# Kernel optimization log

Hardware: AMD Instinct MI355X
Metric: run time of the kernel (lower is better)

## Reference

```python
import jax, jax.numpy as jnp
import numpy as np

N_CHANNEL = 64
N_BAND = 5
N_CLASS = 2
B = 64
K = 2 * N_CHANNEL  # nodes covered by the fully-connected edge_index


def _w(key, shape):
    fan_in = shape[0] if len(shape) == 2 else int(np.prod(shape[1:]))
    return (jax.random.normal(key, shape, jnp.float32) / np.float32(np.sqrt(fan_in)))


def setup_inputs() -> dict:
    key = jax.random.key(0)
    ks = jax.random.split(key, 22)
    d = {}
    d['x1'] = jax.random.normal(ks[0], (B, K, N_BAND), jnp.float32)
    d['x2'] = jax.random.normal(ks[1], (B, K, K), jnp.float32)
    # GCNConv params (weights stored (in, out); PyG applies linear then aggregates, bias after)
    d['gcn1_w'] = _w(ks[2], (N_BAND, 2 * N_BAND))
    d['gcn1_b'] = 0.01 * jax.random.normal(ks[3], (2 * N_BAND,), jnp.float32)
    d['gcn2_w'] = _w(ks[4], (2 * N_BAND, 1))
    d['gcn2_b'] = 0.01 * jax.random.normal(ks[5], (1,), jnp.float32)
    d['fcg_w'] = _w(ks[6], (K, K))
    d['fcg_b'] = 0.01 * jax.random.normal(ks[7], (K,), jnp.float32)
    d['conv1_w'] = _w(ks[8], (16, 1, 3, 3))   # OIHW
    d['conv1_b'] = 0.01 * jax.random.normal(ks[9], (16,), jnp.float32)
    d['conv2_w'] = _w(ks[10], (16, 16, 3, 3))
    d['conv2_b'] = 0.01 * jax.random.normal(ks[11], (16,), jnp.float32)
    d['fcc_w'] = _w(ks[12], (16 * K * K, K))
    d['fcc_b'] = 0.01 * jax.random.normal(ks[13], (K,), jnp.float32)
    d['fc1_w'] = _w(ks[14], (4 * N_CHANNEL, 2 * N_CHANNEL))
    d['fc1_b'] = 0.01 * jax.random.normal(ks[15], (2 * N_CHANNEL,), jnp.float32)
    d['fc2_w'] = _w(ks[16], (2 * N_CHANNEL, N_CHANNEL))
    d['fc2_b'] = 0.01 * jax.random.normal(ks[17], (N_CHANNEL,), jnp.float32)
    d['fc3_w'] = _w(ks[18], (N_CHANNEL, N_CLASS))
    d['fc3_b'] = 0.01 * jax.random.normal(ks[19], (N_CLASS,), jnp.float32)
    return d


def _gcn(x, W, b):
    # Faithful to original: edge_index is fully connected over the FIRST K rows only.
    # With default self-loops, normalized adjacency over rows [0,K) is (1/K)*ones(K,K)
    # (all degrees = K); every other row has only its self-loop (degree 1 -> identity).
    y = x @ W                                   # (B*N, out)
    y = y.at[:K].set(jnp.mean(y[:K], axis=0))   # broadcast mean over first K rows
    return y + b


def _conv(x, w, b):
    y = jax.lax.conv_general_dilated(x, w, (1, 1), 'SAME',
                                     dimension_numbers=('NCHW', 'OIHW', 'NCHW'))
    return jax.nn.relu(y + b[None, :, None, None])


def reference(x1, x2, gcn1_w, gcn1_b, gcn2_w, gcn2_b, fcg_w, fcg_b,
              conv1_w, conv1_b, conv2_w, conv2_b, fcc_w, fcc_b,
              fc1_w, fc1_b, fc2_w, fc2_b, fc3_w, fc3_b):
    Bn, N, Feat = x1.shape
    # GNN branch (dropout is identity in eval mode)
    h = x1.reshape(Bn * N, Feat)
    h = jax.nn.relu(_gcn(h, gcn1_w, gcn1_b))
    h = jax.nn.relu(_gcn(h, gcn2_w, gcn2_b))
    h = h.reshape(Bn, -1)                       # (B, 2*n_channel)
    g = jax.nn.relu(h @ fcg_w + fcg_b)
    # CNN branch
    c = x2[:, None]                             # (B,1,H,W)
    c = _conv(c, conv1_w, conv1_b)
    c = _conv(c, conv2_w, conv2_b)
    c = c.reshape(Bn, -1)                       # channel-major flatten, same as torch .view
    c = jax.nn.relu(c @ fcc_w + fcc_b)
    # Fusion MLP
    x = jnp.concatenate([c, g], axis=1)
    x = jax.nn.relu(x @ fc1_w + fc1_b)
    x = jax.nn.relu(x @ fc2_w + fc2_b)
    return jax.nn.sigmoid(x @ fc3_w + fc3_b)
```

## Files before the change

kernel.cpp:

```cpp
#include <hip/hip_runtime.h>
#include <hip/hip_bf16.h>


#define NROWS   8192
#define IMG     16384
#define FCC_K   262144
#define FCC_BLOCKS 512
#define FCC_KRANGE 512
#define FCC_CHUNK 128

typedef __attribute__((ext_vector_type(8))) short bf16x8;
typedef __attribute__((ext_vector_type(4))) float f32x4;
typedef __attribute__((ext_vector_type(4))) unsigned short us4;
typedef __attribute__((ext_vector_type(8))) unsigned short us8;

__device__ __forceinline__ unsigned short f2bf(float f) {
    unsigned u = __float_as_uint(f);
    unsigned r = (u + 0x7FFFu + ((u >> 16) & 1u)) >> 16;
    return (unsigned short)r;
}

__device__ __forceinline__ int fcc_swz(int col, int k) {
    return col*128 + (k ^ ((((col >> 2) ^ col) & 15) << 3));
}

__global__ __launch_bounds__(128) void gcnfcg_kernel(
    const float* __restrict__ x1,
    const float* __restrict__ W1,
    const float* __restrict__ b1,
    const float* __restrict__ W2,
    const float* __restrict__ b2,
    const float* __restrict__ fcgW,
    const float* __restrict__ fcgb,
    float* __restrict__ g)
{
    __shared__ float sW1[50], sb1[10], sW2[10], smean[10];
    __shared__ float sy1[128][10];
    __shared__ float sh2[128];
    int b = blockIdx.x, t = threadIdx.x;
    if (t < 50) sW1[t] = W1[t];
    if (t < 10) { sb1[t] = b1[t]; sW2[t] = W2[t]; }
    __syncthreads();

    int r = b*128 + t;
    float x[5];
    #pragma unroll
    for (int f = 0; f < 5; ++f) x[f] = x1[r*5 + f];
    float y[10];
    #pragma unroll
    for (int o = 0; o < 10; ++o) {
        float a = 0.f;
        #pragma unroll
        for (int f = 0; f < 5; ++f) a += x[f] * sW1[f*10 + o];
        y[o] = a;
    }

    float h1row[10];
    if (b == 0) {
        #pragma unroll
        for (int o = 0; o < 10; ++o) sy1[t][o] = y[o];
        __syncthreads();
        if (t < 10) {
            float s = 0.f;
            for (int rr = 0; rr < 128; ++rr) s += sy1[rr][t];
            smean[t] = fmaxf(s * (1.f/128.f) + sb1[t], 0.f);
        }
        __syncthreads();
        #pragma unroll
        for (int o = 0; o < 10; ++o) h1row[o] = smean[o];
    } else {
        #pragma unroll
        for (int o = 0; o < 10; ++o) h1row[o] = fmaxf(y[o] + sb1[o], 0.f);
    }

    float y2 = 0.f;
    #pragma unroll
    for (int o = 0; o < 10; ++o) y2 += h1row[o] * sW2[o];
    sh2[t] = fmaxf(y2 + b2[0], 0.f);
    __syncthreads();

    float acc = fcgb[t];
    #pragma unroll 8
    for (int k = 0; k < 128; ++k) acc += sh2[k] * fcgW[k*128 + t];
    g[b*128 + t] = fmaxf(acc, 0.f);
}

__global__ __launch_bounds__(256) void conv12_kernel(
    const float* __restrict__ x2,
    const float* __restrict__ w1,
    const float* __restrict__ b1,
    const float* __restrict__ w2,
    const float* __restrict__ b2,
    unsigned short* __restrict__ c2bf)
{
    __shared__ float sx2[8][130];
    __shared__ unsigned short sin[6*130*16];
    __shared__ unsigned short sB[5*512];
    __shared__ float sw1[144], sb1v[16];

    int tid = threadIdx.x;
    int blk = blockIdx.x;
    int b   = blk >> 5;
    int R0  = (blk & 31) * 4;

    if (tid < 144) sw1[tid] = w1[tid];
    if (tid < 16)  sb1v[tid] = b1[tid];

    for (int idx = tid; idx < 2560; idx += 256) {
        int q   = idx >> 9;
        int rem = idx & 511;
        int l   = rem >> 3;
        int e   = rem & 7;
        int k   = (l >> 4) * 8 + e;
        int oc  = l & 15;
        int ic  = k & 15;
        int dd  = 2*q + (k >> 4);
        unsigned short bits = 0;
        if (dd < 9) bits = f2bf(w2[oc*144 + ic*9 + dd]);
        sB[idx] = bits;
    }
    if (tid < 192) {
        int rr = tid >> 5, rem = tid & 31;
        int cc = (rem < 16) ? 0 : 129;
        sin[(rr*130 + cc)*16 + (rem & 15)] = 0;
    }
    {
        const float* xb = x2 + (size_t)b * IMG;
        for (int idx = tid; idx < 8*130; idx += 256) {
            int rr = idx / 130, cc = idx - rr*130;
            int ri = R0 - 2 + rr, gj = cc - 1;
            float v = 0.f;
            if (ri >= 0 && ri < 128 && gj >= 0 && gj < 128)
                v = xb[ri*128 + gj];
            sx2[rr][cc] = v;
        }
    }
    __syncthreads();

    for (int p = tid; p < 768; p += 256) {
        int rr = p >> 7;
        int cc = p & 127;
        int ri1 = R0 - 1 + rr;
        bool valid = (ri1 >= 0 && ri1 < 128);
        float in9[3][3];
        #pragma unroll
        for (int di = 0; di < 3; ++di)
          #pragma unroll
          for (int dj = 0; dj < 3; ++dj)
              in9[di][dj] = sx2[rr + di][cc + dj];
        us8 o0, o1;
        #pragma unroll
        for (int oc = 0; oc < 16; ++oc) {
            float acc = sb1v[oc];
            #pragma unroll
            for (int di = 0; di < 3; ++di)
              #pragma unroll
              for (int dj = 0; dj < 3; ++dj)
                  acc += in9[di][dj] * sw1[oc*9 + di*3 + dj];
            unsigned short bits = valid ? f2bf(fmaxf(acc, 0.f)) : (unsigned short)0;
            if (oc < 8) o0[oc] = bits; else o1[oc - 8] = bits;
        }
        unsigned short* dst = &sin[(rr*130 + cc + 1)*16];
        *reinterpret_cast<us8*>(dst)     = o0;
        *reinterpret_cast<us8*>(dst + 8) = o1;
    }
    __syncthreads();

    int lane = tid & 63;
    int wv   = tid >> 6;
    int ln   = lane & 15;
    int g    = lane >> 4;
    int ghalf = g & 1;

    int aoff[5];
    #pragma unroll
    for (int q = 0; q < 5; ++q) {
        int dd = 2*q + (g >> 1);
        if (dd > 8) dd = 8;
        int di = dd / 3, dj = dd % 3;
        aoff[q] = ((wv + di)*130 + ln + dj)*16 + ghalf*8;
    }

    bf16x8 bf[5];
    #pragma unroll
    for (int q = 0; q < 5; ++q)
        bf[q] = *reinterpret_cast<const bf16x8*>(&sB[q*512 + lane*8]);

    float bias_oc = b2[ln];
    int r = R0 + wv;
    unsigned short* outbase = c2bf + ((size_t)b*16 + ln)*IMG + r*128;

    #pragma unroll
    for (int t = 0; t < 8; ++t) {
        f32x4 acc = {0.f, 0.f, 0.f, 0.f};
        #pragma unroll
        for (int q = 0; q < 5; ++q) {
            bf16x8 a = *reinterpret_cast<const bf16x8*>(&sin[aoff[q] + t*256]);
            acc = __builtin_amdgcn_mfma_f32_16x16x32_bf16(a, bf[q], acc, 0, 0, 0);
        }
        int pc = t*16 + g*4;
        us4 pk;
        #pragma unroll
        for (int reg = 0; reg < 4; ++reg)
            pk[reg] = f2bf(fmaxf(acc[reg] + bias_oc, 0.f));
        *reinterpret_cast<us4*>(&outbase[pc]) = pk;
    }
}

__global__ __launch_bounds__(256, 3) void fcc_mfma(
    const unsigned short* __restrict__ c2bf,
    const float* __restrict__ W,
    float* __restrict__ partials)
{
    __shared__ unsigned short sWt[128*128];

    int tid  = threadIdx.x;
    int blk  = blockIdx.x;
    int k0   = blk * FCC_KRANGE;
    int lane = tid & 63, wv = tid >> 6;
    int ln   = lane & 15, g = lane >> 4;

    int q  = tid & 31;
    int kO = tid >> 5;

    f32x4 acc[8];
    #pragma unroll
    for (int j = 0; j < 8; ++j) acc[j] = (f32x4){0.f,0.f,0.f,0.f};

    const float* Wb = W + (size_t)k0 * 128;
    const unsigned short* arow = c2bf + (size_t)(16*wv + ln)*FCC_K + k0 + g*8;

    for (int ci = 0; ci < 4; ++ci) {
        const float* Wc = Wb + (size_t)ci * FCC_CHUNK * 128;
        #pragma unroll
        for (int ko2 = 0; ko2 < 2; ++ko2) {
            int kbase = ko2*64 + kO*8;
            float4 rows[8];
            #pragma unroll
            for (int r = 0; r < 8; ++r)
                rows[r] = *reinterpret_cast<const float4*>(
                    Wc + (size_t)(kbase + r)*128 + q*4);
            us8 vc0, vc1, vc2, vc3;
            #pragma unroll
            for (int r = 0; r < 8; ++r) {
                vc0[r] = f2bf(rows[r].x);
                vc1[r] = f2bf(rows[r].y);
                vc2[r] = f2bf(rows[r].z);
                vc3[r] = f2bf(rows[r].w);
            }
            int col0 = q*4;
            *reinterpret_cast<us8*>(&sWt[fcc_swz(col0+0, kbase)]) = vc0;
            *reinterpret_cast<us8*>(&sWt[fcc_swz(col0+1, kbase)]) = vc1;
            *reinterpret_cast<us8*>(&sWt[fcc_swz(col0+2, kbase)]) = vc2;
            *reinterpret_cast<us8*>(&sWt[fcc_swz(col0+3, kbase)]) = vc3;
        }
        __syncthreads();

        bf16x8 af[4];
        #pragma unroll
        for (int ks = 0; ks < 4; ++ks)
            af[ks] = *reinterpret_cast<const bf16x8*>(arow + ci*FCC_CHUNK + ks*32);

        #pragma unroll
        for (int ks = 0; ks < 4; ++ks) {
            #pragma unroll
            for (int j = 0; j < 8; ++j) {
                int col = j*16 + ln;
                bf16x8 bfrag = *reinterpret_cast<const bf16x8*>(
                    &sWt[fcc_swz(col, ks*32 + g*8)]);
                acc[j] = __builtin_amdgcn_mfma_f32_16x16x32_bf16(af[ks], bfrag, acc[j], 0, 0, 0);
            }
        }
        __syncthreads();
    }

    float* p = partials + (size_t)blk * 8192;
    #pragma unroll
    for (int j = 0; j < 8; ++j)
      #pragma unroll
      for (int reg = 0; reg < 4; ++reg) {
          int m = 16*wv + g*4 + reg;
          p[m*128 + j*16 + ln] = acc[j][reg];
      }
}

__global__ __launch_bounds__(512) void head_kernel(
    const float* __restrict__ partials,
    const float* __restrict__ fccb,
    const float* __restrict__ g,
    const float* __restrict__ w1, const float* __restrict__ bb1,
    const float* __restrict__ w2, const float* __restrict__ bb2,
    const float* __restrict__ w3, const float* __restrict__ bb3,
    float* __restrict__ out)
{
    __shared__ float sred[4][128];
    __shared__ float sx[256], sh[128], s2[64];
    int b = blockIdx.x, t = threadIdx.x;
    int o = t & 127, pr = t >> 7;

    const float* pb = partials + (size_t)pr*8192 + (size_t)b*128 + o;
    float s = 0.f;
    #pragma unroll 8
    for (int p = 0; p < FCC_BLOCKS/4; ++p) s += pb[(size_t)p*4*8192];
    sred[pr][o] = s;
    __syncthreads();

    if (t < 128) {
        sx[t] = fmaxf(sred[0][t] + sred[1][t] + sred[2][t] + sred[3][t]
                      + fccb[t], 0.f);
    } else if (t < 256) {
        sx[t] = g[b*128 + (t - 128)];
    }
    __syncthreads();

    if (t < 128) {
        float acc = bb1[t];
        for (int k = 0; k < 256; ++k) acc += sx[k] * w1[k*128 + t];
        sh[t] = fmaxf(acc, 0.f);
    }
    __syncthreads();
    if (t < 64) {
        float acc = bb2[t];
        for (int k = 0; k < 128; ++k) acc += sh[k] * w2[k*64 + t];
        s2[t] = fmaxf(acc, 0.f);
    }
    __syncthreads();
    if (t < 2) {
        float acc = bb3[t];
        for (int k = 0; k < 64; ++k) acc += s2[k] * w3[k*2 + t];
        out[b*2 + t] = 1.f / (1.f + __expf(-acc));
    }
}

extern "C" void kernel_launch(void* const* d_in, const int* in_sizes, int n_in,
                              void* d_out, int out_size, void* d_ws, size_t ws_size,
                              hipStream_t stream)
{
    const float* x1      = (const float*)d_in[0];
    const float* x2      = (const float*)d_in[1];
    const float* gcn1_w  = (const float*)d_in[2];
    const float* gcn1_b  = (const float*)d_in[3];
    const float* gcn2_w  = (const float*)d_in[4];
    const float* gcn2_b  = (const float*)d_in[5];
    const float* fcg_w   = (const float*)d_in[6];
    const float* fcg_b   = (const float*)d_in[7];
    const float* conv1_w = (const float*)d_in[8];
    const float* conv1_b = (const float*)d_in[9];
    const float* conv2_w = (const float*)d_in[10];
    const float* conv2_b = (const float*)d_in[11];
    const float* fcc_w   = (const float*)d_in[12];
    const float* fcc_b   = (const float*)d_in[13];
    const float* fc1_w   = (const float*)d_in[14];
    const float* fc1_b   = (const float*)d_in[15];
    const float* fc2_w   = (const float*)d_in[16];
    const float* fc2_b   = (const float*)d_in[17];
    const float* fc3_w   = (const float*)d_in[18];
    const float* fc3_b   = (const float*)d_in[19];
    float* out = (float*)d_out;

    float* ws = (float*)d_ws;
    float* g        = ws;
    unsigned short* c2bf = (unsigned short*)(g + 8192);
    float* partials = (float*)(c2bf + 16777216);

    gcnfcg_kernel<<<64, 128, 0, stream>>>(x1, gcn1_w, gcn1_b, gcn2_w, gcn2_b,
                                          fcg_w, fcg_b, g);
    conv12_kernel<<<2048, 256, 0, stream>>>(x2, conv1_w, conv1_b,
                                            conv2_w, conv2_b, c2bf);
    fcc_mfma<<<FCC_BLOCKS, 256, 0, stream>>>(c2bf, fcc_w, partials);
    head_kernel<<<64, 512, 0, stream>>>(partials, fcc_b, g, fc1_w, fc1_b,
                                        fc2_w, fc2_b, fc3_w, fc3_b, out);
}
```

Measured before the change: 96.22 us.

## Double-buffer fcc weight tiles and fold GCN branch into head kernel

The fcc GEMM kernel now processes 64-row chunks with two shared-memory buffers. Each iteration issues the global loads of the next chunk's weights and activations before running the MFMAs on the current chunk, so memory latency overlaps compute. Occupancy is lowered to 2 blocks per CU. Separately, the GCN+fcg kernel is removed and its work is fused into the head kernel, saving one launch and a workspace round trip at the cost of a longer head kernel.

```diff
diff --git a/kernel.cpp b/kernel.cpp
--- a/kernel.cpp
+++ b/kernel.cpp
@@ -7,7 +7,8 @@
 #define FCC_K   262144
 #define FCC_BLOCKS 512
 #define FCC_KRANGE 512
-#define FCC_CHUNK 128
+#define FCC_CHUNK 64
+#define FCC_NCHUNK 8
 
 typedef __attribute__((ext_vector_type(8))) short bf16x8;
 typedef __attribute__((ext_vector_type(4))) float f32x4;
@@ -20,69 +21,8 @@
     return (unsigned short)r;
 }
 
-__device__ __forceinline__ int fcc_swz(int col, int k) {
-    return col*128 + (k ^ ((((col >> 2) ^ col) & 15) << 3));
-}
-
-__global__ __launch_bounds__(128) void gcnfcg_kernel(
-    const float* __restrict__ x1,
-    const float* __restrict__ W1,
-    const float* __restrict__ b1,
-    const float* __restrict__ W2,
-    const float* __restrict__ b2,
-    const float* __restrict__ fcgW,
-    const float* __restrict__ fcgb,
-    float* __restrict__ g)
-{
-    __shared__ float sW1[50], sb1[10], sW2[10], smean[10];
-    __shared__ float sy1[128][10];
-    __shared__ float sh2[128];
-    int b = blockIdx.x, t = threadIdx.x;
-    if (t < 50) sW1[t] = W1[t];
-    if (t < 10) { sb1[t] = b1[t]; sW2[t] = W2[t]; }
-    __syncthreads();
-
-    int r = b*128 + t;
-    float x[5];
-    #pragma unroll
-    for (int f = 0; f < 5; ++f) x[f] = x1[r*5 + f];
-    float y[10];
-    #pragma unroll
-    for (int o = 0; o < 10; ++o) {
-        float a = 0.f;
-        #pragma unroll
-        for (int f = 0; f < 5; ++f) a += x[f] * sW1[f*10 + o];
-        y[o] = a;
-    }
-
-    float h1row[10];
-    if (b == 0) {
-        #pragma unroll
-        for (int o = 0; o < 10; ++o) sy1[t][o] = y[o];
-        __syncthreads();
-        if (t < 10) {
-            float s = 0.f;
-            for (int rr = 0; rr < 128; ++rr) s += sy1[rr][t];
-            smean[t] = fmaxf(s * (1.f/128.f) + sb1[t], 0.f);
-        }
-        __syncthreads();
-        #pragma unroll
-        for (int o = 0; o < 10; ++o) h1row[o] = smean[o];
-    } else {
-        #pragma unroll
-        for (int o = 0; o < 10; ++o) h1row[o] = fmaxf(y[o] + sb1[o], 0.f);
-    }
-
-    float y2 = 0.f;
-    #pragma unroll
-    for (int o = 0; o < 10; ++o) y2 += h1row[o] * sW2[o];
-    sh2[t] = fmaxf(y2 + b2[0], 0.f);
-    __syncthreads();
-
-    float acc = fcgb[t];
-    #pragma unroll 8
-    for (int k = 0; k < 128; ++k) acc += sh2[k] * fcgW[k*128 + t];
-    g[b*128 + t] = fmaxf(acc, 0.f);
+__device__ __forceinline__ int fcc_swz64(int col, int k) {
+    return col*64 + (k ^ ((((col >> 2) ^ col) & 7) << 3));
 }
 
 __global__ __launch_bounds__(256) void conv12_kernel(
@@ -207,21 +147,20 @@
     }
 }
 
-__global__ __launch_bounds__(256, 3) void fcc_mfma(
+__global__ __launch_bounds__(256, 2) void fcc_mfma(
     const unsigned short* __restrict__ c2bf,
     const float* __restrict__ W,
     float* __restrict__ partials)
 {
-    __shared__ unsigned short sWt[128*128];
+    __shared__ unsigned short sWt[2][FCC_CHUNK*128];
 
     int tid  = threadIdx.x;
     int blk  = blockIdx.x;
     int k0   = blk * FCC_KRANGE;
     int lane = tid & 63, wv = tid >> 6;
     int ln   = lane & 15, g = lane >> 4;
-
-    int q  = tid & 31;
-    int kO = tid >> 5;
+    int q    = tid & 31;
+    int kO   = tid >> 5;
 
     f32x4 acc[8];
     #pragma unroll
@@ -229,47 +168,68 @@
 
     const float* Wb = W + (size_t)k0 * 128;
     const unsigned short* arow = c2bf + (size_t)(16*wv + ln)*FCC_K + k0 + g*8;
-
-    for (int ci = 0; ci < 4; ++ci) {
-        const float* Wc = Wb + (size_t)ci * FCC_CHUNK * 128;
-        #pragma unroll
-        for (int ko2 = 0; ko2 < 2; ++ko2) {
-            int kbase = ko2*64 + kO*8;
-            float4 rows[8];
+    int col0 = q*4;
+
+    float4 rows[8];
+    bf16x8 afc0, afc1, afn0, afn1;
+
+    #pragma unroll
+    for (int r = 0; r < 8; ++r)
+        rows[r] = *reinterpret_cast<const float4*>(
+            Wb + (size_t)(kO*8 + r)*128 + col0);
+    afc0 = *reinterpret_cast<const bf16x8*>(arow);
+    afc1 = *reinterpret_cast<const bf16x8*>(arow + 32);
+    {
+        us8 vc0, vc1, vc2, vc3;
+        #pragma unroll
+        for (int r = 0; r < 8; ++r) {
+            vc0[r] = f2bf(rows[r].x); vc1[r] = f2bf(rows[r].y);
+            vc2[r] = f2bf(rows[r].z); vc3[r] = f2bf(rows[r].w);
+        }
+        *reinterpret_cast<us8*>(&sWt[0][fcc_swz64(col0+0, kO*8)]) = vc0;
+        *reinterpret_cast<us8*>(&sWt[0][fcc_swz64(col0+1, kO*8)]) = vc1;
+        *reinterpret_cast<us8*>(&sWt[0][fcc_swz64(col0+2, kO*8)]) = vc2;
+        *reinterpret_cast<us8*>(&sWt[0][fcc_swz64(col0+3, kO*8)]) = vc3;
+    }
+    __syncthreads();
+
+    for (int ci = 0; ci < FCC_NCHUNK; ++ci) {
+        const unsigned short* bufC = &sWt[ci & 1][0];
+        if (ci < FCC_NCHUNK-1) {
+            const float* Wc = Wb + (size_t)(ci + 1) * FCC_CHUNK * 128;
             #pragma unroll
             for (int r = 0; r < 8; ++r)
                 rows[r] = *reinterpret_cast<const float4*>(
-                    Wc + (size_t)(kbase + r)*128 + q*4);
+                    Wc + (size_t)(kO*8 + r)*128 + col0);
+            afn0 = *reinterpret_cast<const bf16x8*>(arow + (ci+1)*FCC_CHUNK);
+            afn1 = *reinterpret_cast<const bf16x8*>(arow + (ci+1)*FCC_CHUNK + 32);
+        }
+        #pragma unroll
+        for (int j = 0; j < 8; ++j) {
+            bf16x8 bfrag = *reinterpret_cast<const bf16x8*>(
+                &bufC[fcc_swz64(j*16 + ln, g*8)]);
+            acc[j] = __builtin_amdgcn_mfma_f32_16x16x32_bf16(afc0, bfrag, acc[j], 0, 0, 0);
+        }
+        #pragma unroll
+        for (int j = 0; j < 8; ++j) {
+            bf16x8 bfrag = *reinterpret_cast<const bf16x8*>(
+                &bufC[fcc_swz64(j*16 + ln, 32 + g*8)]);
+            acc[j] = __builtin_amdgcn_mfma_f32_16x16x32_bf16(afc1, bfrag, acc[j], 0, 0, 0);
+        }
+        __syncthreads();
+        if (ci < FCC_NCHUNK-1) {
+            unsigned short* bufN = &sWt[(ci + 1) & 1][0];
             us8 vc0, vc1, vc2, vc3;
             #pragma unroll
             for (int r = 0; r < 8; ++r) {
-                vc0[r] = f2bf(rows[r].x);
-                vc1[r] = f2bf(rows[r].y);
-                vc2[r] = f2bf(rows[r].z);
-                vc3[r] = f2bf(rows[r].w);
+                vc0[r] = f2bf(rows[r].x); vc1[r] = f2bf(rows[r].y);
+                vc2[r] = f2bf(rows[r].z); vc3[r] = f2bf(rows[r].w);
             }
-            int col0 = q*4;
-            *reinterpret_cast<us8*>(&sWt[fcc_swz(col0+0, kbase)]) = vc0;
-            *reinterpret_cast<us8*>(&sWt[fcc_swz(col0+1, kbase)]) = vc1;
-            *reinterpret_cast<us8*>(&sWt[fcc_swz(col0+2, kbase)]) = vc2;
-            *reinterpret_cast<us8*>(&sWt[fcc_swz(col0+3, kbase)]) = vc3;
-        }
-        __syncthreads();
-
-        bf16x8 af[4];
-        #pragma unroll
-        for (int ks = 0; ks < 4; ++ks)
-            af[ks] = *reinterpret_cast<const bf16x8*>(arow + ci*FCC_CHUNK + ks*32);
-
-        #pragma unroll
-        for (int ks = 0; ks < 4; ++ks) {
-            #pragma unroll
-            for (int j = 0; j < 8; ++j) {
-                int col = j*16 + ln;
-                bf16x8 bfrag = *reinterpret_cast<const bf16x8*>(
-                    &sWt[fcc_swz(col, ks*32 + g*8)]);
-                acc[j] = __builtin_amdgcn_mfma_f32_16x16x32_bf16(af[ks], bfrag, acc[j], 0, 0, 0);
-            }
+            *reinterpret_cast<us8*>(&bufN[fcc_swz64(col0+0, kO*8)]) = vc0;
+            *reinterpret_cast<us8*>(&bufN[fcc_swz64(col0+1, kO*8)]) = vc1;
+            *reinterpret_cast<us8*>(&bufN[fcc_swz64(col0+2, kO*8)]) = vc2;
+            *reinterpret_cast<us8*>(&bufN[fcc_swz64(col0+3, kO*8)]) = vc3;
+            afc0 = afn0; afc1 = afn1;
         }
         __syncthreads();
     }
@@ -287,29 +247,88 @@
 __global__ __launch_bounds__(512) void head_kernel(
     const float* __restrict__ partials,
     const float* __restrict__ fccb,
-    const float* __restrict__ g,
+    const float* __restrict__ x1,
+    const float* __restrict__ gW1,
+    const float* __restrict__ gb1,
+    const float* __restrict__ gW2,
+    const float* __restrict__ gb2,
+    const float* __restrict__ fcgW,
+    const float* __restrict__ fcgb,
     const float* __restrict__ w1, const float* __restrict__ bb1,
     const float* __restrict__ w2, const float* __restrict__ bb2,
     const float* __restrict__ w3, const float* __restrict__ bb3,
     float* __restrict__ out)
 {
     __shared__ float sred[4][128];
-    __shared__ float sx[256], sh[128], s2[64];
+    __shared__ float sx[256], sh[128], s2[64], sh2[128];
+    __shared__ float sW1[50], sb1s[10], sW2s[10], smean[10];
+    __shared__ float sy1[128][10];
     int b = blockIdx.x, t = threadIdx.x;
     int o = t & 127, pr = t >> 7;
 
-    const float* pb = partials + (size_t)pr*8192 + (size_t)b*128 + o;
-    float s = 0.f;
-    #pragma unroll 8
-    for (int p = 0; p < FCC_BLOCKS/4; ++p) s += pb[(size_t)p*4*8192];
-    sred[pr][o] = s;
-    __syncthreads();
-
-    if (t < 128) {
+    {
+        const float* pb = partials + (size_t)pr*8192 + (size_t)b*128 + o;
+        float s = 0.f;
+        #pragma unroll 8
+        for (int p = 0; p < FCC_BLOCKS/4; ++p) s += pb[(size_t)p*4*8192];
+        sred[pr][o] = s;
+    }
+    if (t < 50) sW1[t] = gW1[t];
+    if (t >= 64 && t < 74) { sb1s[t-64] = gb1[t-64]; sW2s[t-64] = gW2[t-64]; }
+    __syncthreads();
+
+    if (t < 128)
         sx[t] = fmaxf(sred[0][t] + sred[1][t] + sred[2][t] + sred[3][t]
                       + fccb[t], 0.f);
-    } else if (t < 256) {
-        sx[t] = g[b*128 + (t - 128)];
+
+    float y[10];
+    if (t < 128) {
+        int r = b*128 + t;
+        float x[5];
+        #pragma unroll
+        for (int f = 0; f < 5; ++f) x[f] = x1[r*5 + f];
+        #pragma unroll
+        for (int oo = 0; oo < 10; ++oo) {
+            float a = 0.f;
+            #pragma unroll
+            for (int f = 0; f < 5; ++f) a += x[f] * sW1[f*10 + oo];
+            y[oo] = a;
+        }
+    }
+    if (b == 0) {
+        if (t < 128) {
+            #pragma unroll
+            for (int oo = 0; oo < 10; ++oo) sy1[t][oo] = y[oo];
+        }
+        __syncthreads();
+        if (t < 10) {
+            float s = 0.f;
+            for (int rr = 0; rr < 128; ++rr) s += sy1[rr][t];
+            smean[t] = fmaxf(s * (1.f/128.f) + sb1s[t], 0.f);
+        }
+        __syncthreads();
+    }
+    if (t < 128) {
+        float h1row[10];
+        if (b == 0) {
+            #pragma unroll
+            for (int oo = 0; oo < 10; ++oo) h1row[oo] = smean[oo];
+        } else {
+            #pragma unroll
+            for (int oo = 0; oo < 10; ++oo) h1row[oo] = fmaxf(y[oo] + sb1s[oo], 0.f);
+        }
+        float y2 = 0.f;
+        #pragma unroll
+        for (int oo = 0; oo < 10; ++oo) y2 += h1row[oo] * sW2s[oo];
+        sh2[t] = fmaxf(y2 + gb2[0], 0.f);
+    }
+    __syncthreads();
+
+    if (t < 128) {
+        float acc = fcgb[t];
+        #pragma unroll 8
+        for (int k = 0; k < 128; ++k) acc += sh2[k] * fcgW[k*128 + t];
+        sx[128 + t] = fmaxf(acc, 0.f);
     }
     __syncthreads();
 
@@ -358,16 +377,15 @@
     const float* fc3_b   = (const float*)d_in[19];
     float* out = (float*)d_out;
 
-    float* ws = (float*)d_ws;
-    float* g        = ws;
-    unsigned short* c2bf = (unsigned short*)(g + 8192);
+    unsigned short* c2bf = (unsigned short*)d_ws;
     float* partials = (float*)(c2bf + 16777216);
 
-    gcnfcg_kernel<<<64, 128, 0, stream>>>(x1, gcn1_w, gcn1_b, gcn2_w, gcn2_b,
-                                          fcg_w, fcg_b, g);
     conv12_kernel<<<2048, 256, 0, stream>>>(x2, conv1_w, conv1_b,
                                             conv2_w, conv2_b, c2bf);
     fcc_mfma<<<FCC_BLOCKS, 256, 0, stream>>>(c2bf, fcc_w, partials);
-    head_kernel<<<64, 512, 0, stream>>>(partials, fcc_b, g, fc1_w, fc1_b,
-                                        fc2_w, fc2_b, fc3_w, fc3_b, out);
-}
+    head_kernel<<<64, 512, 0, stream>>>(partials, fcc_b,
+                                        x1, gcn1_w, gcn1_b, gcn2_w, gcn2_b,
+                                        fcg_w, fcg_b,
+                                        fc1_w, fc1_b, fc2_w, fc2_b,
+                                        fc3_w, fc3_b, out);
+}
```

Result: faster. 90.25 us (-6.2%).
